# Kernel tuning notes

Measured on AMD Instinct MI355X. Metric: run time of the kernel, lower is better.

Reference implementation:

```python
import jax, jax.numpy as jnp
import numpy as np

# dims (match init_kwargs)
S = 2048      # sequence_length
H = 2048      # hidden_size
NH = 32       # num_attention_heads
KVH = 8       # num_key_value_heads
HD = 64       # head_dim
WIN = 128     # sliding_window
QM = NH // KVH
SM_SCALE = 1.0 / float(np.sqrt(HD))


def _rope_rotate(x, cos, sin):
    # x: [S, n, HD]; cos/sin: [S, HD//2]
    x1, x2 = jnp.split(x, 2, axis=-1)
    c = cos[:, None, :].astype(x.dtype)
    s = sin[:, None, :].astype(x.dtype)
    return jnp.concatenate([x1 * c - x2 * s, x2 * c + x1 * s], axis=-1)


def setup_inputs() -> dict:
    key = jax.random.key(0)
    ks = jax.random.split(key, 6)
    x = jax.random.normal(ks[0], (S, H), jnp.float32)
    qkv_dim = HD * (NH + 2 * KVH)
    qkv_kernel = jax.random.normal(ks[1], (H, qkv_dim), jnp.float32) * 0.02
    qkv_bias = jnp.zeros((qkv_dim,), jnp.float32)
    out_kernel = jax.random.normal(ks[2], (NH * HD, H), jnp.float32) * 0.02
    out_bias = jnp.zeros((H,), jnp.float32)
    sinks = jax.random.normal(ks[3], (NH,), jnp.float32) * 0.02
    # RoPE tables: [S, HD//2]
    pos = np.arange(S, dtype=np.float32)
    inv_freq = 1.0 / (10000.0 ** (np.arange(HD // 2, dtype=np.float32) / (HD // 2)))
    ang = pos[:, None] * inv_freq[None, :]
    cos_table = jnp.asarray(np.cos(ang), jnp.float32)
    sin_table = jnp.asarray(np.sin(ang), jnp.float32)
    # causal + sliding-window additive mask [S, S]
    qi = np.arange(S, dtype=np.int32)[:, None]
    ki = np.arange(S, dtype=np.int32)[None, :]
    m = np.where(ki > qi, -np.inf, 0.0).astype(np.float32)
    m = np.where(ki < qi - WIN, -np.inf, m).astype(np.float32)
    mask = jnp.asarray(m)
    return {"x": x, "qkv_kernel": qkv_kernel, "qkv_bias": qkv_bias,
            "out_kernel": out_kernel, "out_bias": out_bias, "sinks": sinks,
            "cos_table": cos_table, "sin_table": sin_table, "mask": mask}


def reference(x, qkv_kernel, qkv_bias, out_kernel, out_bias, sinks, cos_table, sin_table, mask):
    xf = x.astype(jnp.float32)
    qkv = jnp.dot(xf, qkv_kernel, precision=jax.lax.Precision.HIGHEST) + qkv_bias  # [S, qkv_dim]
    q_end = NH * HD
    k_end = q_end + KVH * HD
    q = qkv[:, :q_end].reshape(S, NH, HD)          # NH = KVH*QM
    k = qkv[:, q_end:k_end].reshape(S, KVH, HD)
    v = qkv[:, k_end:].reshape(S, KVH, HD)
    q = _rope_rotate(q, cos_table, sin_table).reshape(S, KVH, QM, HD)
    k = _rope_rotate(k, cos_table, sin_table)
    # logits: [KVH, QM, S_q, S_k]; K broadcast across q_mult (GQA)
    logits = jnp.einsum('qhmd,khd->hmqk', q, k) * jnp.float32(SM_SCALE)
    logits = logits + mask[None, None, :, :]
    sink = jnp.broadcast_to(sinks.reshape(KVH, QM, 1, 1).astype(jnp.float32), (KVH, QM, S, 1))
    extended = jnp.concatenate([logits, sink], axis=-1)
    weights = jax.nn.softmax(extended, axis=-1)[..., :-1]
    attn = jnp.einsum('hmqk,khd->qhmd', weights, v).reshape(S, NH * HD)
    out = jnp.dot(attn, out_kernel, precision=jax.lax.Precision.HIGHEST) + out_bias
    return out.astype(x.dtype)
```

## Files before the change

### kernel.cpp

```cpp
#include <hip/hip_runtime.h>
#include <hip/hip_bf16.h>
#include <cstdint>

typedef __hip_bfloat16 bf16;
typedef __attribute__((ext_vector_type(8))) __bf16 bf16x8;
typedef __attribute__((ext_vector_type(4))) float f32x4;

static __device__ __forceinline__ void gload_lds16(const void* g, void* l) {
  __builtin_amdgcn_global_load_lds(
      (const __attribute__((address_space(1))) uint32_t*)g,
      (__attribute__((address_space(3))) uint32_t*)l, 16, 0, 0);
}

__global__ __launch_bounds__(256)
void prep_kernel(const float* __restrict__ x, const float* __restrict__ w1,
                 const float* __restrict__ w2, bf16* __restrict__ xb,
                 bf16* __restrict__ w1t, bf16* __restrict__ w2t) {
  __shared__ float tile[32][33];
  const int lin = blockIdx.x;
  const int t = threadIdx.x;
  if (lin < 4096) {
    const int i = lin * 256 + t;
    const float4 v = reinterpret_cast<const float4*>(x)[i];
    ushort4 o;
    o.x = __builtin_bit_cast(unsigned short, __float2bfloat16(v.x));
    o.y = __builtin_bit_cast(unsigned short, __float2bfloat16(v.y));
    o.z = __builtin_bit_cast(unsigned short, __float2bfloat16(v.z));
    o.w = __builtin_bit_cast(unsigned short, __float2bfloat16(v.w));
    reinterpret_cast<ushort4*>(xb)[i] = o;
    return;
  }
  const float* in;
  bf16* out;
  int R, C, bx, by;
  if (lin < 10240) {
    const int tl = lin - 4096;
    in = w1; out = w1t; R = 2048; C = 3072; bx = tl % 96; by = tl / 96;
  } else {
    const int tl = lin - 10240;
    in = w2; out = w2t; R = 2048; C = 2048; bx = tl & 63; by = tl >> 6;
  }
  const int c0 = bx * 32, r0 = by * 32;
  const int tx = t & 31, ty = t >> 5;
#pragma unroll
  for (int i = 0; i < 4; ++i)
    tile[ty + i * 8][tx] = in[(size_t)(r0 + ty + i * 8) * C + c0 + tx];
  __syncthreads();
#pragma unroll
  for (int i = 0; i < 4; ++i)
    out[(size_t)(c0 + ty + i * 8) * R + r0 + tx] = __float2bfloat16(tile[tx][ty + i * 8]);
}

template <int NH, int SSHIFT>
__global__ void rope_kernel(bf16* __restrict__ buf, const float* __restrict__ cosT,
                            const float* __restrict__ sinT) {
  const int idx = blockIdx.x * 256 + threadIdx.x;
  const int c = idx & 3;
  const int h = (idx >> 2) & (NH - 1);
  const int s = idx >> SSHIFT;
  bf16* p = buf + (size_t)s * (NH * 64) + h * 64 + c * 8;
  bf16x8 v1 = *reinterpret_cast<bf16x8*>(p);
  bf16x8 v2 = *reinterpret_cast<bf16x8*>(p + 32);
  const float4 c0 = *reinterpret_cast<const float4*>(&cosT[s * 32 + c * 8]);
  const float4 c1 = *reinterpret_cast<const float4*>(&cosT[s * 32 + c * 8 + 4]);
  const float4 s0 = *reinterpret_cast<const float4*>(&sinT[s * 32 + c * 8]);
  const float4 s1 = *reinterpret_cast<const float4*>(&sinT[s * 32 + c * 8 + 4]);
  const float cs[8] = {c0.x, c0.y, c0.z, c0.w, c1.x, c1.y, c1.z, c1.w};
  const float sn[8] = {s0.x, s0.y, s0.z, s0.w, s1.x, s1.y, s1.z, s1.w};
  bf16x8 o1, o2;
#pragma unroll
  for (int e = 0; e < 8; ++e) {
    const float x1 = (float)v1[e], x2 = (float)v2[e];
    o1[e] = (__bf16)(x1 * cs[e] - x2 * sn[e]);
    o2[e] = (__bf16)(x2 * cs[e] + x1 * sn[e]);
  }
  *reinterpret_cast<bf16x8*>(p) = o1;
  *reinterpret_cast<bf16x8*>(p + 32) = o2;
}

__global__ __launch_bounds__(512, 1)
void gemm1_kernel(const bf16* __restrict__ A, const bf16* __restrict__ Bt,
                  const float* __restrict__ bias,
                  bf16* __restrict__ qb, bf16* __restrict__ kb, bf16* __restrict__ vt) {
  extern __shared__ __align__(16) char smem[];
  constexpr int K = 2048, NK = 32;
  const int lin = blockIdx.x;
  const int wgid = (lin & 7) * 32 + (lin >> 3);
  const int bx = wgid >> 4, by = wgid & 15;
  const int brow = by * 128, bcol = bx * 192;
  const int t = threadIdx.x, lane = t & 63, w = t >> 6;
  const int wr = w >> 2, wc = w & 3;
  const int rr = lane & 15, rg = lane >> 4;

  char* Ab = smem;
  char* Bb = smem + 49152;

  auto stageA = [&](int kt) {
#pragma unroll
    for (int p = 0; p < 2; ++p) {
      const int idx = p * 512 + t;
      const int row = idx >> 3;
      const int cg = (idx & 7) ^ (row & 7);
      gload_lds16(A + (size_t)(brow + row) * K + kt * 64 + cg * 8,
                  Ab + (size_t)(kt % 3) * 16384 + (p * 512 + (t & ~63)) * 16);
    }
  };
  auto stageB = [&](int kt) {
#pragma unroll
    for (int p = 0; p < 3; ++p) {
      const int idx = p * 512 + t;
      const int row = idx >> 3;
      const int cg = (idx & 7) ^ (row & 7);
      gload_lds16(Bt + (size_t)(bcol + row) * K + kt * 64 + cg * 8,
                  Bb + (size_t)(kt % 3) * 24576 + (p * 512 + (t & ~63)) * 16);
    }
  };

  f32x4 acc[4][3];
#pragma unroll
  for (int i = 0; i < 4; ++i)
#pragma unroll
    for (int j = 0; j < 3; ++j) acc[i][j] = f32x4{0.f, 0.f, 0.f, 0.f};

  stageA(0); stageB(0); stageA(1); stageB(1);
  asm volatile("s_waitcnt vmcnt(5)" ::: "memory");
  __builtin_amdgcn_s_barrier();

  for (int kt = 0; kt < NK; ++kt) {
    const char* Ar = Ab + (size_t)(kt % 3) * 16384;
    const char* Br = Bb + (size_t)(kt % 3) * 24576;
#pragma unroll
    for (int ks = 0; ks < 2; ++ks) {
      bf16x8 af[4], bfr[3];
      const int c = ks * 4 + rg;
#pragma unroll
      for (int i = 0; i < 4; ++i) {
        const int row = wr * 64 + i * 16 + rr;
        af[i] = *reinterpret_cast<const bf16x8*>(Ar + row * 128 + ((c ^ (row & 7)) * 16));
      }
#pragma unroll
      for (int j = 0; j < 3; ++j) {
        const int row = wc * 48 + j * 16 + rr;
        bfr[j] = *reinterpret_cast<const bf16x8*>(Br + row * 128 + ((c ^ (row & 7)) * 16));
      }
      if (kt + 2 < NK) {
        if (ks == 0) stageA(kt + 2);
        else         stageB(kt + 2);
      }
      asm volatile("s_waitcnt lgkmcnt(0)" ::: "memory");
      __builtin_amdgcn_sched_barrier(0);
      __builtin_amdgcn_s_setprio(1);
#pragma unroll
      for (int i = 0; i < 4; ++i)
#pragma unroll
        for (int j = 0; j < 3; ++j)
          acc[i][j] = __builtin_amdgcn_mfma_f32_16x16x32_bf16(af[i], bfr[j], acc[i][j], 0, 0, 0);
      __builtin_amdgcn_s_setprio(0);
    }
    if (kt + 2 < NK)      asm volatile("s_waitcnt vmcnt(5)" ::: "memory");
    else if (kt + 1 < NK) asm volatile("s_waitcnt vmcnt(0)" ::: "memory");
    if (kt + 1 < NK) __builtin_amdgcn_s_barrier();
  }

#pragma unroll
  for (int j = 0; j < 3; ++j) {
    const int gcf = bcol + wc * 48 + j * 16;
    const int gc = gcf + rr;
    const float bv = bias[gc];
    if (gcf < 2048) {
#pragma unroll
      for (int i = 0; i < 4; ++i) {
        const int s0 = brow + wr * 64 + i * 16 + rg * 4;
#pragma unroll
        for (int r = 0; r < 4; ++r)
          qb[(size_t)(s0 + r) * 2048 + gc] = __float2bfloat16(acc[i][j][r] + bv);
      }
    } else if (gcf < 2560) {
      const int kc = gc - 2048;
#pragma unroll
      for (int i = 0; i < 4; ++i) {
        const int s0 = brow + wr * 64 + i * 16 + rg * 4;
#pragma unroll
        for (int r = 0; r < 4; ++r)
          kb[(size_t)(s0 + r) * 512 + kc] = __float2bfloat16(acc[i][j][r] + bv);
      }
    } else {
      const int vcol = gc - 2560;
#pragma unroll
      for (int i = 0; i < 4; ++i) {
        ushort4 o;
        o.x = __builtin_bit_cast(unsigned short, __float2bfloat16(acc[i][j][0] + bv));
        o.y = __builtin_bit_cast(unsigned short, __float2bfloat16(acc[i][j][1] + bv));
        o.z = __builtin_bit_cast(unsigned short, __float2bfloat16(acc[i][j][2] + bv));
        o.w = __builtin_bit_cast(unsigned short, __float2bfloat16(acc[i][j][3] + bv));
        *reinterpret_cast<ushort4*>(
            &vt[(size_t)vcol * 2048 + brow + wr * 64 + i * 16 + rg * 4]) = o;
      }
    }
  }
}

__global__ __launch_bounds__(512, 1)
void gemm2_kernel(const bf16* __restrict__ A, const bf16* __restrict__ Bt,
                  const float* __restrict__ bias, float* __restrict__ C) {
  extern __shared__ __align__(16) char smem[];
  constexpr int K = 2048, NK = 32;
  const int lin = blockIdx.x;
  const int wgid = (lin & 7) * 32 + (lin >> 3);
  const int bx = wgid >> 4, by = wgid & 15;
  const int brow = by * 128, bcol = bx * 128;
  const int t = threadIdx.x, lane = t & 63, w = t >> 6;
  const int wr = (w & 3) >> 1, wc = w & 1, khalf = w >> 2;
  const int rr = lane & 15, rg = lane >> 4;

  char* Ab = smem;
  char* Bb = smem + 49152;

  auto stage = [&](int kt) {
#pragma unroll
    for (int p = 0; p < 2; ++p) {
      const int idx = p * 512 + t;
      const int row = idx >> 3;
      const int cg = (idx & 7) ^ (row & 7);
      gload_lds16(A + (size_t)(brow + row) * K + kt * 64 + cg * 8,
                  Ab + (size_t)(kt % 3) * 16384 + (p * 512 + (t & ~63)) * 16);
      gload_lds16(Bt + (size_t)(bcol + row) * K + kt * 64 + cg * 8,
                  Bb + (size_t)(kt % 3) * 16384 + (p * 512 + (t & ~63)) * 16);
    }
  };

  f32x4 acc[4][4];
#pragma unroll
  for (int i = 0; i < 4; ++i)
#pragma unroll
    for (int j = 0; j < 4; ++j) acc[i][j] = f32x4{0.f, 0.f, 0.f, 0.f};

  stage(0); stage(1);
  asm volatile("s_waitcnt vmcnt(4)" ::: "memory");
  __builtin_amdgcn_s_barrier();

  for (int kt = 0; kt < NK; ++kt) {
    const char* Ar = Ab + (size_t)(kt % 3) * 16384;
    const char* Br = Bb + (size_t)(kt % 3) * 16384;
    bf16x8 af[4], bfr[4];
    const int c = khalf * 4 + rg;
#pragma unroll
    for (int i = 0; i < 4; ++i) {
      const int row = wr * 64 + i * 16 + rr;
      af[i] = *reinterpret_cast<const bf16x8*>(Ar + row * 128 + ((c ^ (row & 7)) * 16));
    }
#pragma unroll
    for (int j = 0; j < 4; ++j) {
      const int row = wc * 64 + j * 16 + rr;
      bfr[j] = *reinterpret_cast<const bf16x8*>(Br + row * 128 + ((c ^ (row & 7)) * 16));
    }
    if (kt + 2 < NK) stage(kt + 2);
    asm volatile("s_waitcnt lgkmcnt(0)" ::: "memory");
    __builtin_amdgcn_sched_barrier(0);
    __builtin_amdgcn_s_setprio(1);
#pragma unroll
    for (int i = 0; i < 4; ++i)
#pragma unroll
      for (int j = 0; j < 4; ++j)
        acc[i][j] = __builtin_amdgcn_mfma_f32_16x16x32_bf16(af[i], bfr[j], acc[i][j], 0, 0, 0);
    __builtin_amdgcn_s_setprio(0);
    if (kt + 2 < NK)      asm volatile("s_waitcnt vmcnt(4)" ::: "memory");
    else if (kt + 1 < NK) asm volatile("s_waitcnt vmcnt(0)" ::: "memory");
    if (kt + 1 < NK) __builtin_amdgcn_s_barrier();
  }

  __syncthreads();
  float* red = (float*)smem;
  if (w >= 4) {
#pragma unroll
    for (int i = 0; i < 4; ++i)
#pragma unroll
      for (int j = 0; j < 4; ++j)
        *reinterpret_cast<f32x4*>(&red[(w - 4) * 4096 + (i * 4 + j) * 256 + lane * 4]) = acc[i][j];
  }
  __syncthreads();
  if (w < 4) {
#pragma unroll
    for (int i = 0; i < 4; ++i)
#pragma unroll
      for (int j = 0; j < 4; ++j) {
        const f32x4 o = *reinterpret_cast<const f32x4*>(&red[w * 4096 + (i * 4 + j) * 256 + lane * 4]);
        const int gc = bcol + wc * 64 + j * 16 + rr;
        const float bv = bias[gc];
        const int r0 = brow + wr * 64 + i * 16 + rg * 4;
#pragma unroll
        for (int r = 0; r < 4; ++r)
          C[(size_t)(r0 + r) * 2048 + gc] = acc[i][j][r] + o[r] + bv;
      }
  }
}

__global__ __launch_bounds__(256, 2)
void attn_kernel(const bf16* __restrict__ Q, const bf16* __restrict__ Kb,
                 const bf16* __restrict__ Vt, const float* __restrict__ sinks,
                 const float* __restrict__ cosT, const float* __restrict__ sinT,
                 bf16* __restrict__ aout) {
  extern __shared__ __align__(16) char smem[];
  const int hk = blockIdx.x;
  const int q0 = blockIdx.y * 32;
  const int k0 = q0 - 128;
  const int t = threadIdx.x, w = t >> 6, lane = t & 63;
  const int cl = lane & 15, rg = lane >> 4;
  const int head = hk * 4 + w;

  char* Ks = smem;
  char* Ps = smem + 20480 + w * 12288;

#pragma unroll
  for (int p = 0; p < 5; ++p) {
    const int idx = p * 256 + t;
    const int row = idx >> 3, c = idx & 7;
    int key = k0 + row;
    if (key < 0) key = 0;
    gload_lds16(Kb + (size_t)key * 512 + hk * 64 + ((c ^ (row & 7)) << 3),
                Ks + (size_t)(p * 256 + (t & ~63)) * 16);
  }

  bf16x8 aq[2][2];
#pragma unroll
  for (int qf = 0; qf < 2; ++qf) {
    const int qrow = q0 + qf * 16 + cl;
    const bf16* qp = Q + (size_t)qrow * 2048 + head * 64 + rg * 8;
    const bf16x8 q1 = *reinterpret_cast<const bf16x8*>(qp);
    const bf16x8 q2 = *reinterpret_cast<const bf16x8*>(qp + 32);
    const float4 c0 = *reinterpret_cast<const float4*>(&cosT[qrow * 32 + rg * 8]);
    const float4 c1 = *reinterpret_cast<const float4*>(&cosT[qrow * 32 + rg * 8 + 4]);
    const float4 s0 = *reinterpret_cast<const float4*>(&sinT[qrow * 32 + rg * 8]);
    const float4 s1 = *reinterpret_cast<const float4*>(&sinT[qrow * 32 + rg * 8 + 4]);
    const float cs[8] = {c0.x, c0.y, c0.z, c0.w, c1.x, c1.y, c1.z, c1.w};
    const float sn[8] = {s0.x, s0.y, s0.z, s0.w, s1.x, s1.y, s1.z, s1.w};
#pragma unroll
    for (int e = 0; e < 8; ++e) {
      const float x1 = (float)q1[e], x2 = (float)q2[e];
      aq[qf][0][e] = (__bf16)(x1 * cs[e] - x2 * sn[e]);
      aq[qf][1][e] = (__bf16)(x2 * cs[e] + x1 * sn[e]);
    }
  }
  __syncthreads();

  f32x4 acc[2][10];
#pragma unroll
  for (int qf = 0; qf < 2; ++qf)
#pragma unroll
    for (int nf = 0; nf < 10; ++nf) acc[qf][nf] = f32x4{0.f, 0.f, 0.f, 0.f};

#pragma unroll
  for (int nf = 0; nf < 10; ++nf) {
    const int row = nf * 16 + cl;
    bf16x8 bk[2];
#pragma unroll
    for (int ks = 0; ks < 2; ++ks) {
      const int chunk = ks * 4 + rg;
      bk[ks] = *reinterpret_cast<const bf16x8*>(
          Ks + row * 128 + ((chunk ^ (row & 7)) << 4));
    }
#pragma unroll
    for (int qf = 0; qf < 2; ++qf)
#pragma unroll
      for (int ks = 0; ks < 2; ++ks)
        acc[qf][nf] = __builtin_amdgcn_mfma_f32_16x16x32_bf16(aq[qf][ks], bk[ks], acc[qf][nf], 0, 0, 0);
  }

  const float sinkv = sinks[head];
  const float scale = 0.125f;
  const int cfloor = 128 - q0;
#pragma unroll
  for (int qf = 0; qf < 2; ++qf)
#pragma unroll
    for (int r = 0; r < 4; ++r) {
      const int rowb = qf * 16 + rg * 4 + r;
      int cmin = rowb;
      if (cfloor > cmin) cmin = cfloor;
      const int cmax = rowb + 128;
      float m = sinkv;
      float pv[10];
#pragma unroll
      for (int nf = 0; nf < 10; ++nf) {
        const int cc = nf * 16 + cl;
        float lv = (cc >= cmin && cc <= cmax) ? acc[qf][nf][r] * scale : -INFINITY;
        pv[nf] = lv;
        m = fmaxf(m, lv);
      }
#pragma unroll
      for (int off = 1; off < 16; off <<= 1)
        m = fmaxf(m, __shfl_xor(m, off, 64));
      float sum = 0.f;
#pragma unroll
      for (int nf = 0; nf < 10; ++nf) {
        const float p = __expf(pv[nf] - m);
        pv[nf] = p;
        sum += p;
      }
#pragma unroll
      for (int off = 1; off < 16; off <<= 1)
        sum += __shfl_xor(sum, off, 64);
      sum += __expf(sinkv - m);
      const float inv = 1.f / sum;
#pragma unroll
      for (int nf = 0; nf < 10; ++nf) {
        const int col = nf * 16 + cl;
        const int chunk = col >> 3;
        *reinterpret_cast<bf16*>(Ps + rowb * 384 + ((chunk ^ (rowb & 7)) << 4) + (cl & 7) * 2) =
            __float2bfloat16(pv[nf] * inv);
      }
    }

  asm volatile("s_waitcnt lgkmcnt(0)" ::: "memory");
  __builtin_amdgcn_sched_barrier(0);

  f32x4 oacc[2][4];
#pragma unroll
  for (int qf = 0; qf < 2; ++qf)
#pragma unroll
    for (int j = 0; j < 4; ++j) oacc[qf][j] = f32x4{0.f, 0.f, 0.f, 0.f};

#pragma unroll
  for (int ks = 0; ks < 5; ++ks) {
    bf16x8 pa[2];
#pragma unroll
    for (int qf = 0; qf < 2; ++qf) {
      const int row = qf * 16 + cl;
      const int chunk = ks * 4 + rg;
      pa[qf] = *reinterpret_cast<const bf16x8*>(
          Ps + row * 384 + ((chunk ^ (row & 7)) << 4));
    }
    int key = k0 + ks * 32 + rg * 8;
    if (key < 0) key = 0;
#pragma unroll
    for (int j = 0; j < 4; ++j) {
      const bf16x8 bv = *reinterpret_cast<const bf16x8*>(
          Vt + ((size_t)hk * 64 + j * 16 + cl) * 2048 + key);
#pragma unroll
      for (int qf = 0; qf < 2; ++qf)
        oacc[qf][j] = __builtin_amdgcn_mfma_f32_16x16x32_bf16(pa[qf], bv, oacc[qf][j], 0, 0, 0);
    }
  }

#pragma unroll
  for (int qf = 0; qf < 2; ++qf)
#pragma unroll
    for (int j = 0; j < 4; ++j)
#pragma unroll
      for (int r = 0; r < 4; ++r) {
        const int gr = q0 + qf * 16 + rg * 4 + r;
        const int gc = head * 64 + j * 16 + cl;
        aout[(size_t)gr * 2048 + gc] = __float2bfloat16(oacc[qf][j][r]);
      }
}

extern "C" void kernel_launch(void* const* d_in, const int* in_sizes, int n_in,
                              void* d_out, int out_size, void* d_ws, size_t ws_size,
                              hipStream_t stream) {
  const float* x     = (const float*)d_in[0];
  const float* w1    = (const float*)d_in[1];
  const float* b1    = (const float*)d_in[2];
  const float* w2    = (const float*)d_in[3];
  const float* b2    = (const float*)d_in[4];
  const float* sinks = (const float*)d_in[5];
  const float* cosT  = (const float*)d_in[6];
  const float* sinT  = (const float*)d_in[7];
  float* out = (float*)d_out;

  char* ws = (char*)d_ws;
  bf16* xb   = (bf16*)(ws);
  bf16* w1t  = (bf16*)(ws + 8388608);
  bf16* w2t  = (bf16*)(ws + 20971520);
  bf16* qbuf = (bf16*)(ws + 29360128);
  bf16* kbuf = (bf16*)(ws + 37748736);
  bf16* vt   = (bf16*)(ws + 39845888);
  bf16* attn = (bf16*)(ws + 41943040);
  (void)in_sizes; (void)n_in; (void)out_size; (void)ws_size;

  prep_kernel<<<14336, 256, 0, stream>>>(x, w1, w2, xb, w1t, w2t);
  gemm1_kernel<<<256, 512, 122880, stream>>>(xb, w1t, b1, qbuf, kbuf, vt);
  rope_kernel<8, 5><<<256, 256, 0, stream>>>(kbuf, cosT, sinT);
  attn_kernel<<<dim3(8, 64), 256, 69632, stream>>>(qbuf, kbuf, vt, sinks, cosT, sinT, attn);
  gemm2_kernel<<<256, 512, 98304, stream>>>(attn, w2t, b2, out);
}
```

Baseline: 86.72 us.

## Split LDS fragment waits to overlap MFMA with reads and prefetch V early

In both GEMM kernels the next-tile global-to-LDS staging is issued at the top of each iteration. The LDS fragment reads are then split into two groups with partial lgkmcnt waits, so the first batch of MFMAs can start while the remaining fragment loads are still in flight. In the attention kernel, all V fragments are loaded from global memory into registers before the softmax, so their latency hides behind the softmax math. The cost is higher register pressure, which may lower occupancy, and the partial waits depend on the exact LDS instruction counts being right.

```diff
diff --git a/kernel.cpp b/kernel.cpp
--- a/kernel.cpp
+++ b/kernel.cpp
@@ -129,34 +129,41 @@
   for (int kt = 0; kt < NK; ++kt) {
     const char* Ar = Ab + (size_t)(kt % 3) * 16384;
     const char* Br = Bb + (size_t)(kt % 3) * 24576;
+    if (kt + 2 < NK) { stageA(kt + 2); stageB(kt + 2); }
+    bf16x8 af[2][4], bfr[2][3];
 #pragma unroll
     for (int ks = 0; ks < 2; ++ks) {
-      bf16x8 af[4], bfr[3];
       const int c = ks * 4 + rg;
 #pragma unroll
       for (int i = 0; i < 4; ++i) {
         const int row = wr * 64 + i * 16 + rr;
-        af[i] = *reinterpret_cast<const bf16x8*>(Ar + row * 128 + ((c ^ (row & 7)) * 16));
+        af[ks][i] = *reinterpret_cast<const bf16x8*>(Ar + row * 128 + ((c ^ (row & 7)) * 16));
       }
 #pragma unroll
       for (int j = 0; j < 3; ++j) {
         const int row = wc * 48 + j * 16 + rr;
-        bfr[j] = *reinterpret_cast<const bf16x8*>(Br + row * 128 + ((c ^ (row & 7)) * 16));
-      }
-      if (kt + 2 < NK) {
-        if (ks == 0) stageA(kt + 2);
-        else         stageB(kt + 2);
-      }
-      asm volatile("s_waitcnt lgkmcnt(0)" ::: "memory");
-      __builtin_amdgcn_sched_barrier(0);
-      __builtin_amdgcn_s_setprio(1);
-#pragma unroll
-      for (int i = 0; i < 4; ++i)
-#pragma unroll
-        for (int j = 0; j < 3; ++j)
-          acc[i][j] = __builtin_amdgcn_mfma_f32_16x16x32_bf16(af[i], bfr[j], acc[i][j], 0, 0, 0);
-      __builtin_amdgcn_s_setprio(0);
-    }
+        bfr[ks][j] = *reinterpret_cast<const bf16x8*>(Br + row * 128 + ((c ^ (row & 7)) * 16));
+      }
+      if (ks == 0) __builtin_amdgcn_sched_barrier(0);
+    }
+    asm volatile("s_waitcnt lgkmcnt(7)" ::: "memory");
+    __builtin_amdgcn_sched_barrier(0);
+    __builtin_amdgcn_s_setprio(1);
+#pragma unroll
+    for (int i = 0; i < 4; ++i)
+#pragma unroll
+      for (int j = 0; j < 3; ++j)
+        acc[i][j] = __builtin_amdgcn_mfma_f32_16x16x32_bf16(af[0][i], bfr[0][j], acc[i][j], 0, 0, 0);
+    __builtin_amdgcn_s_setprio(0);
+    asm volatile("s_waitcnt lgkmcnt(0)" ::: "memory");
+    __builtin_amdgcn_sched_barrier(0);
+    __builtin_amdgcn_s_setprio(1);
+#pragma unroll
+    for (int i = 0; i < 4; ++i)
+#pragma unroll
+      for (int j = 0; j < 3; ++j)
+        acc[i][j] = __builtin_amdgcn_mfma_f32_16x16x32_bf16(af[1][i], bfr[1][j], acc[i][j], 0, 0, 0);
+    __builtin_amdgcn_s_setprio(0);
     if (kt + 2 < NK)      asm volatile("s_waitcnt vmcnt(5)" ::: "memory");
     else if (kt + 1 < NK) asm volatile("s_waitcnt vmcnt(0)" ::: "memory");
     if (kt + 1 < NK) __builtin_amdgcn_s_barrier();
@@ -242,19 +249,39 @@
   for (int kt = 0; kt < NK; ++kt) {
     const char* Ar = Ab + (size_t)(kt % 3) * 16384;
     const char* Br = Bb + (size_t)(kt % 3) * 16384;
+    if (kt + 2 < NK) stage(kt + 2);
     bf16x8 af[4], bfr[4];
     const int c = khalf * 4 + rg;
 #pragma unroll
-    for (int i = 0; i < 4; ++i) {
+    for (int i = 0; i < 2; ++i) {
       const int row = wr * 64 + i * 16 + rr;
       af[i] = *reinterpret_cast<const bf16x8*>(Ar + row * 128 + ((c ^ (row & 7)) * 16));
     }
 #pragma unroll
-    for (int j = 0; j < 4; ++j) {
+    for (int j = 0; j < 2; ++j) {
       const int row = wc * 64 + j * 16 + rr;
       bfr[j] = *reinterpret_cast<const bf16x8*>(Br + row * 128 + ((c ^ (row & 7)) * 16));
     }
-    if (kt + 2 < NK) stage(kt + 2);
+    __builtin_amdgcn_sched_barrier(0);
+#pragma unroll
+    for (int i = 2; i < 4; ++i) {
+      const int row = wr * 64 + i * 16 + rr;
+      af[i] = *reinterpret_cast<const bf16x8*>(Ar + row * 128 + ((c ^ (row & 7)) * 16));
+    }
+#pragma unroll
+    for (int j = 2; j < 4; ++j) {
+      const int row = wc * 64 + j * 16 + rr;
+      bfr[j] = *reinterpret_cast<const bf16x8*>(Br + row * 128 + ((c ^ (row & 7)) * 16));
+    }
+    asm volatile("s_waitcnt lgkmcnt(4)" ::: "memory");
+    __builtin_amdgcn_sched_barrier(0);
+    __builtin_amdgcn_s_setprio(1);
+#pragma unroll
+    for (int i = 0; i < 2; ++i)
+#pragma unroll
+      for (int j = 0; j < 2; ++j)
+        acc[i][j] = __builtin_amdgcn_mfma_f32_16x16x32_bf16(af[i], bfr[j], acc[i][j], 0, 0, 0);
+    __builtin_amdgcn_s_setprio(0);
     asm volatile("s_waitcnt lgkmcnt(0)" ::: "memory");
     __builtin_amdgcn_sched_barrier(0);
     __builtin_amdgcn_s_setprio(1);
@@ -262,7 +289,8 @@
     for (int i = 0; i < 4; ++i)
 #pragma unroll
       for (int j = 0; j < 4; ++j)
-        acc[i][j] = __builtin_amdgcn_mfma_f32_16x16x32_bf16(af[i], bfr[j], acc[i][j], 0, 0, 0);
+        if (i >= 2 || j >= 2)
+          acc[i][j] = __builtin_amdgcn_mfma_f32_16x16x32_bf16(af[i], bfr[j], acc[i][j], 0, 0, 0);
     __builtin_amdgcn_s_setprio(0);
     if (kt + 2 < NK)      asm volatile("s_waitcnt vmcnt(4)" ::: "memory");
     else if (kt + 1 < NK) asm volatile("s_waitcnt vmcnt(0)" ::: "memory");
@@ -366,6 +394,17 @@
         acc[qf][nf] = __builtin_amdgcn_mfma_f32_16x16x32_bf16(aq[qf][ks], bk[ks], acc[qf][nf], 0, 0, 0);
   }
 
+  bf16x8 vb[5][4];
+#pragma unroll
+  for (int ks = 0; ks < 5; ++ks) {
+    int key = k0 + ks * 32 + rg * 8;
+    if (key < 0) key = 0;
+#pragma unroll
+    for (int j = 0; j < 4; ++j)
+      vb[ks][j] = *reinterpret_cast<const bf16x8*>(
+          Vt + ((size_t)hk * 64 + j * 16 + cl) * 2048 + key);
+  }
+
   const float sinkv = sinks[head];
   const float scale = 0.125f;
   const int cfloor = 128 - q0;
@@ -429,16 +468,11 @@
       pa[qf] = *reinterpret_cast<const bf16x8*>(
           Ps + row * 384 + ((chunk ^ (row & 7)) << 4));
     }
-    int key = k0 + ks * 32 + rg * 8;
-    if (key < 0) key = 0;
-#pragma unroll
-    for (int j = 0; j < 4; ++j) {
-      const bf16x8 bv = *reinterpret_cast<const bf16x8*>(
-          Vt + ((size_t)hk * 64 + j * 16 + cl) * 2048 + key);
+#pragma unroll
+    for (int j = 0; j < 4; ++j)
 #pragma unroll
       for (int qf = 0; qf < 2; ++qf)
-        oacc[qf][j] = __builtin_amdgcn_mfma_f32_16x16x32_bf16(pa[qf], bv, oacc[qf][j], 0, 0, 0);
-    }
+        oacc[qf][j] = __builtin_amdgcn_mfma_f32_16x16x32_bf16(pa[qf], vb[ks][j], oacc[qf][j], 0, 0, 0);
   }
 
 #pragma unroll
```

Result: no change. 88.46 us (+2.0%).
